# Performance work log

Hardware: AMD Instinct MI355X
Metric: run time of the kernel (lower is better)

The kernel has to match this reference:

```python
import jax, jax.numpy as jnp
import numpy as np
from jax import lax

TOP_K = 4
ROUTED_SCALING = 1.0
RENORMALIZE = True


def setup_inputs() -> dict:
    key = jax.random.key(0)
    ks = jax.random.split(key, 9)
    H, I, E = 2048, 1024, 16
    s = 0.02
    return {
        "hidden_states": jax.random.normal(ks[0], (2, 1024, H), jnp.float32),
        "gate_w": jax.random.normal(ks[1], (E, H), jnp.float32) * s,
        "expert_bias": jax.random.normal(ks[2], (E,), jnp.float32) * s,
        "w_gate": jax.random.normal(ks[3], (E, I, H), jnp.float32) * s,
        "w_up": jax.random.normal(ks[4], (E, I, H), jnp.float32) * s,
        "w_down": jax.random.normal(ks[5], (E, H, I), jnp.float32) * s,
        "sw_gate": jax.random.normal(ks[6], (I, H), jnp.float32) * s,
        "sw_up": jax.random.normal(ks[7], (I, H), jnp.float32) * s,
        "sw_down": jax.random.normal(ks[8], (H, I), jnp.float32) * s,
    }


def _swiglu_ffn(x, wg, wu, wd):
    # SiluAndMul(gate_up) -> down_proj
    return (jax.nn.silu(x @ wg.T) * (x @ wu.T)) @ wd.T


def reference(hidden_states, gate_w, expert_bias, w_gate, w_up, w_down,
              sw_gate, sw_up, sw_down):
    orig_shape = hidden_states.shape
    H = orig_shape[-1]
    x = hidden_states.reshape(-1, H)            # [T, H]
    T = x.shape[0]

    # --- sigmoid gating with score-correction bias (bias affects selection only) ---
    logits = x.astype(jnp.float32) @ gate_w.T    # [T, E] fp32 router
    scores = jax.nn.sigmoid(logits)
    _, topk_idx = lax.top_k(scores + expert_bias[None, :], TOP_K)   # [T, K]
    topk_w = jnp.take_along_axis(scores, topk_idx, axis=-1)         # raw scores
    if RENORMALIZE:
        topk_w = topk_w / jnp.sum(topk_w, axis=-1, keepdims=True)
    topk_w = topk_w * ROUTED_SCALING

    # scatter top-k weights into dense [T, E] combine matrix
    E = gate_w.shape[0]
    combine = jnp.zeros((T, E), dtype=x.dtype).at[
        jnp.arange(T)[:, None], topk_idx].set(topk_w.astype(x.dtype))

    # --- routed experts: scan over experts, weighted accumulate ---
    def step(acc, ws):
        wg, wu, wd, cw = ws                     # cw: [T] combine weights
        return acc + cw[:, None] * _swiglu_ffn(x, wg, wu, wd), None

    routed, _ = lax.scan(step, jnp.zeros_like(x),
                         (w_gate, w_up, w_down, combine.T))

    # --- shared expert ---
    shared = _swiglu_ffn(x, sw_gate, sw_up, sw_down)

    return (routed + shared).reshape(orig_shape)
```

## Files before the change

kernel.cpp:

```cpp
#include <hip/hip_runtime.h>
#include <hip/hip_bf16.h>
#include <cstdint>

#define TK 2048
#define HD 2048
#define ID 1024
#define NE 16
#define NG 17
#define TOPK 4
#define SLOTS (TK*TOPK)
#define ROWS_ALL (SLOTS+TK)
#define IH (ID*HD)
#define MAXT 96
#define MAXTR 80

typedef __attribute__((ext_vector_type(4))) float f32x4;
typedef __attribute__((ext_vector_type(16))) float f32x16;
typedef __attribute__((ext_vector_type(8))) short s16x8;
typedef unsigned short u16;
typedef unsigned long long u64;

__device__ __forceinline__ u16 f2bf(float f){
  union { float f; uint32_t u; } v; v.f = f;
  uint32_t r = v.u + 0x7fffu + ((v.u >> 16) & 1u);
  return (u16)(r >> 16);
}

#define GLD16(g, l) __builtin_amdgcn_global_load_lds( \
    (const __attribute__((address_space(1))) void*)(g), \
    (__attribute__((address_space(3))) void*)(l), 16, 0, 0)

__device__ __forceinline__ const s16x8* fragp(const u16* b, int row, int off){
  return (const s16x8*)((const char*)b + row*128 + (off ^ ((row&7)<<4)));
}

#define MFMA32(a,b,c) __builtin_amdgcn_mfma_f32_32x32x16_bf16((a),(b),(c),0,0,0)

__global__ void k_prep(const float* __restrict__ x, u16* __restrict__ xb,
                       u64* __restrict__ maskbits){
  int gi = blockIdx.x*blockDim.x + threadIdx.x;
  int st = gridDim.x*blockDim.x;
  if (gi < NE*32) maskbits[gi] = 0ull;
  for (int i=gi; i<TK*HD/4; i+=st){
    float4 f = ((const float4*)x)[i];
    ushort4 o; o.x=f2bf(f.x); o.y=f2bf(f.y); o.z=f2bf(f.z); o.w=f2bf(f.w);
    ((ushort4*)xb)[i] = o;
  }
}

__global__ void k_cvtw(const float* __restrict__ wg, const float* __restrict__ wu,
                       const float* __restrict__ wd, const float* __restrict__ swg,
                       const float* __restrict__ swu, const float* __restrict__ swd,
                       u16* __restrict__ wgb, u16* __restrict__ wub, u16* __restrict__ wdb){
  const size_t nbig = (size_t)NE*IH/4, nsml = IH/4;
  const size_t total = 3*nbig + 3*nsml;
  for (size_t i = (size_t)blockIdx.x*blockDim.x + threadIdx.x; i < total;
       i += (size_t)gridDim.x*blockDim.x){
    const float4* src; ushort4* dst; size_t j = i;
    if (j < nbig){ src=(const float4*)wg + j;  dst=(ushort4*)wgb + j; }
    else if ((j-=nbig) < nbig){ src=(const float4*)wu + j;  dst=(ushort4*)wub + j; }
    else if ((j-=nbig) < nbig){ src=(const float4*)wd + j;  dst=(ushort4*)wdb + j; }
    else if ((j-=nbig) < nsml){ src=(const float4*)swg + j; dst=(ushort4*)wgb + nbig + j; }
    else if ((j-=nsml) < nsml){ src=(const float4*)swu + j; dst=(ushort4*)wub + nbig + j; }
    else { j-=nsml; src=(const float4*)swd + j; dst=(ushort4*)wdb + nbig + j; }
    float4 f = *src;
    ushort4 o; o.x=f2bf(f.x); o.y=f2bf(f.y); o.z=f2bf(f.z); o.w=f2bf(f.w);
    *dst = o;
  }
}

__global__ __launch_bounds__(256) void k_logits(const float* __restrict__ x,
                                                const float* __restrict__ gw,
                                                const float* __restrict__ bias,
                                                float* __restrict__ wdense,
                                                u64* __restrict__ maskbits){
  int t = blockIdx.x, tid = threadIdx.x;
  int lane = tid & 63, wv = tid >> 6;
  const float* xr = x + (size_t)t*HD;
  float acc[NE];
  #pragma unroll
  for (int e=0;e<NE;e++) acc[e]=0.f;
  for (int k=tid;k<HD;k+=256){
    float xv = xr[k];
    #pragma unroll
    for (int e=0;e<NE;e++) acc[e] += xv * gw[e*HD + k];
  }
  __shared__ float red[NE][4];
  #pragma unroll
  for (int e=0;e<NE;e++){
    float v = acc[e];
    #pragma unroll
    for (int off=32;off>0;off>>=1) v += __shfl_down(v, off, 64);
    if (lane==0) red[e][wv] = v;
  }
  __syncthreads();
  if (tid == 0){
    float sc[NE], bs[NE];
    #pragma unroll
    for (int e=0;e<NE;e++){
      float l = red[e][0]+red[e][1]+red[e][2]+red[e][3];
      float s = 1.f/(1.f+expf(-l));
      sc[e]=s; bs[e]=s+bias[e];
    }
    int idx[TOPK]; float wsum=0.f; unsigned used=0;
    for (int k=0;k<TOPK;k++){
      int best=0; float bv=-1e30f;
      for (int e=0;e<NE;e++) if (!((used>>e)&1u) && bs[e] > bv){ bv=bs[e]; best=e; }
      used |= 1u<<best; idx[k]=best; wsum += sc[best];
    }
    float inv = 1.f/wsum;
    for (int k=0;k<TOPK;k++){
      int e = idx[k];
      wdense[t*NE + e] = sc[e]*inv;
      atomicOr(&maskbits[e*32 + (t>>6)], 1ull << (t&63));
    }
  }
}

__global__ void k_scan(const u64* __restrict__ maskbits, int* __restrict__ counts,
                       int* __restrict__ offsets, int* __restrict__ wordpfx,
                       int* __restrict__ tiles, int* __restrict__ tilesR){
  int acc = 0;
  for (int e=0;e<NE;e++){
    int c = 0;
    for (int w=0;w<32;w++){ wordpfx[e*32+w] = c; c += __popcll(maskbits[e*32+w]); }
    counts[e] = c;
  }
  for (int e=0;e<NE;e++){ offsets[e] = acc; acc += counts[e]; }
  offsets[NE] = acc;
  counts[NE] = TK;
  int nt = 0, nr = 0;
  for (int g=0; g<NG; g++){
    int c = counts[g];
    for (int mt=0; mt*128 < c; mt++){
      if (nt < MAXT) tiles[nt++] = (g<<8) | mt;
      if (g < NE && nr < MAXTR) tilesR[nr++] = (g<<8) | mt;
    }
  }
  for (; nt<MAXT;  nt++) tiles[nt]  = -1;
  for (; nr<MAXTR; nr++) tilesR[nr] = -1;
}

__global__ void k_scatter(const u64* __restrict__ maskbits, const int* __restrict__ offsets,
                          const int* __restrict__ wordpfx, const float* __restrict__ wdense,
                          int* __restrict__ rowtok, float* __restrict__ roww){
  int t = blockIdx.x*blockDim.x + threadIdx.x;
  int e = blockIdx.y;
  if (t >= TK) return;
  if (e == NE){ rowtok[offsets[NE]+t] = t; roww[offsets[NE]+t] = 1.f; return; }
  u64 w = maskbits[e*32 + (t>>6)];
  if ((w >> (t&63)) & 1ull){
    int pos = offsets[e] + wordpfx[e*32 + (t>>6)] + __popcll(w & ((1ull << (t&63)) - 1ull));
    rowtok[pos] = t; roww[pos] = wdense[t*NE + e];
  }
}

__global__ __launch_bounds__(256, 2) void k_gemm1b(
    const u16* __restrict__ xb, const u16* __restrict__ wgb, const u16* __restrict__ wub,
    const int* __restrict__ counts, const int* __restrict__ offsets,
    const int* __restrict__ rowtok, const float* __restrict__ roww,
    const int* __restrict__ tiles, u16* __restrict__ P)
{
  int te = tiles[blockIdx.y];
  if (te < 0) return;
  int g = te >> 8, mt = te & 255;
  int cnt = counts[g];
  int n0 = blockIdx.x*128;
  int base = offsets[g];
  const u16* wg16 = wgb + (size_t)g*IH;
  const u16* wu16 = wub + (size_t)g*IH;

  __shared__ u16 lsA[128*64];
  __shared__ u16 lsG[128*64];
  __shared__ u16 lsU[128*64];

  int tid = threadIdx.x, lane = tid & 63, wv = tid >> 6;
  int wm = (wv>>1)*64, wn64 = (wv&1)*64;
  int rl = lane & 31, hi = lane >> 5;

  f32x16 accg[2][2] = {}; f32x16 accu[2][2] = {};

  const u16 *aSrc[4], *gSrc[4], *uSrc[4];
  #pragma unroll
  for (int i=0;i<4;i++){
    int b = i*256 + tid, r = b>>3, cb = b&7;
    int m = mt*128 + r; if (m >= cnt) m = cnt-1;
    int tok = rowtok[base + m];
    aSrc[i] = xb + (size_t)tok*HD + ((cb ^ (r&7))<<3);
    size_t woff = (size_t)(n0 + r)*HD + ((cb ^ (r&7))<<3);
    gSrc[i] = wg16 + woff; uSrc[i] = wu16 + woff;
  }

  for (int t=0; t<HD/64; ++t){
    int k0 = t*64;
    #pragma unroll
    for (int i=0;i<4;i++) GLD16(aSrc[i]+k0, lsA + (i*256 + wv*64)*8);
    #pragma unroll
    for (int i=0;i<4;i++) GLD16(gSrc[i]+k0, lsG + (i*256 + wv*64)*8);
    #pragma unroll
    for (int i=0;i<4;i++) GLD16(uSrc[i]+k0, lsU + (i*256 + wv*64)*8);
    asm volatile("s_waitcnt vmcnt(0)" ::: "memory");
    __builtin_amdgcn_s_barrier();
    #pragma unroll
    for (int s=0; s<4; ++s){
      int off = s*32 + hi*16;
      s16x8 af[2], bg[2], bu[2];
      af[0] = *fragp(lsA, wm + rl, off);
      af[1] = *fragp(lsA, wm + 32 + rl, off);
      bg[0] = *fragp(lsG, wn64 + rl, off);
      bg[1] = *fragp(lsG, wn64 + 32 + rl, off);
      bu[0] = *fragp(lsU, wn64 + rl, off);
      bu[1] = *fragp(lsU, wn64 + 32 + rl, off);
      #pragma unroll
      for (int mi=0;mi<2;mi++){
        #pragma unroll
        for (int j=0;j<2;j++){
          accg[mi][j] = MFMA32(af[mi], bg[j], accg[mi][j]);
          accu[mi][j] = MFMA32(af[mi], bu[j], accu[mi][j]);
        }
      }
    }
    asm volatile("s_waitcnt lgkmcnt(0)" ::: "memory");
    __builtin_amdgcn_s_barrier();
  }
  #pragma unroll
  for (int mi=0;mi<2;mi++){
    #pragma unroll
    for (int r=0;r<16;r++){
      int rowb = wm + mi*32 + (r&3) + 8*(r>>2) + 4*hi;
      int m = mt*128 + rowb;
      if (m < cnt){
        int slot = base + m;
        float wgt = roww[slot];
        #pragma unroll
        for (int j=0;j<2;j++){
          float gv = accg[mi][j][r], uv = accu[mi][j][r];
          float pv = gv/(1.f+expf(-gv))*uv*wgt;
          P[(size_t)slot*ID + n0 + wn64 + j*32 + rl] = f2bf(pv);
        }
      }
    }
  }
}

template<bool ATOMIC>
__global__ __launch_bounds__(256, 2) void k_gemm2b(
    const u16* __restrict__ P, const u16* __restrict__ wdb,
    const int* __restrict__ counts, const int* __restrict__ offsets,
    const int* __restrict__ rowtok, const int* __restrict__ tiles,
    float* __restrict__ out)
{
  int g, mt, cnt, base;
  if (ATOMIC){
    int te = tiles[blockIdx.y];
    if (te < 0) return;
    g = te >> 8; mt = te & 255; cnt = counts[g]; base = offsets[g];
  } else {
    g = NE; mt = blockIdx.y; cnt = TK; base = SLOTS;
  }
  int n0 = blockIdx.x*256;
  const u16* wd16 = wdb + (size_t)g*IH;

  __shared__ u16 lsA[128*64];
  __shared__ u16 lsB[256*64];

  int tid = threadIdx.x, lane = tid & 63, wv = tid >> 6;
  int wm = (wv>>1)*64, wn = (wv&1)*128;
  int rl = lane & 31, hi = lane >> 5;
  f32x16 acc[2][4] = {};

  const u16* aSrc[4];
  #pragma unroll
  for (int i=0;i<4;i++){
    int b = i*256 + tid, r = b>>3, cb = b&7;
    int m = mt*128 + r; if (m >= cnt) m = cnt-1;
    aSrc[i] = P + (size_t)(base + m)*ID + ((cb ^ (r&7))<<3);
  }
  const u16* bSrc[8];
  #pragma unroll
  for (int i=0;i<8;i++){
    int b = i*256 + tid, r = b>>3, cb = b&7;
    bSrc[i] = wd16 + (size_t)(n0 + r)*ID + ((cb ^ (r&7))<<3);
  }

  for (int t=0; t<ID/64; ++t){
    int k0 = t*64;
    #pragma unroll
    for (int i=0;i<4;i++) GLD16(aSrc[i]+k0, lsA + (i*256 + wv*64)*8);
    #pragma unroll
    for (int i=0;i<8;i++) GLD16(bSrc[i]+k0, lsB + (i*256 + wv*64)*8);
    asm volatile("s_waitcnt vmcnt(0)" ::: "memory");
    __builtin_amdgcn_s_barrier();
    #pragma unroll
    for (int s=0; s<4; ++s){
      int off = s*32 + hi*16;
      s16x8 af[2], bf[4];
      af[0] = *fragp(lsA, wm + rl, off);
      af[1] = *fragp(lsA, wm + 32 + rl, off);
      #pragma unroll
      for (int nj=0;nj<4;nj++) bf[nj] = *fragp(lsB, wn + nj*32 + rl, off);
      #pragma unroll
      for (int mi=0;mi<2;mi++)
        #pragma unroll
        for (int nj=0;nj<4;nj++)
          acc[mi][nj] = MFMA32(af[mi], bf[nj], acc[mi][nj]);
    }
    asm volatile("s_waitcnt lgkmcnt(0)" ::: "memory");
    __builtin_amdgcn_s_barrier();
  }
  #pragma unroll
  for (int mi=0;mi<2;mi++){
    #pragma unroll
    for (int r=0;r<16;r++){
      int rowb = wm + mi*32 + (r&3) + 8*(r>>2) + 4*hi;
      int m = mt*128 + rowb;
      if (m < cnt){
        int tok = rowtok[base + m];
        float* orow = out + (size_t)tok*HD + n0 + wn + rl;
        #pragma unroll
        for (int nj=0;nj<4;nj++){
          if (ATOMIC) atomicAdd(orow + nj*32, acc[mi][nj][r]);
          else        orow[nj*32] = acc[mi][nj][r];
        }
      }
    }
  }
}


extern "C" void kernel_launch(void* const* d_in, const int* in_sizes, int n_in,
                              void* d_out, int out_size, void* d_ws, size_t ws_size,
                              hipStream_t stream){
  (void)in_sizes; (void)n_in; (void)ws_size; (void)out_size;
  const float* x       = (const float*)d_in[0];
  const float* gate_w  = (const float*)d_in[1];
  const float* ebias   = (const float*)d_in[2];
  const float* w_gate  = (const float*)d_in[3];
  const float* w_up    = (const float*)d_in[4];
  const float* w_down  = (const float*)d_in[5];
  const float* sw_gate = (const float*)d_in[6];
  const float* sw_up   = (const float*)d_in[7];
  const float* sw_down = (const float*)d_in[8];
  float* out = (float*)d_out;

  char* p = (char*)d_ws;
  auto alloc = [&](size_t bytes)->char*{ char* r = p; p += (bytes + 255) & ~(size_t)255; return r; };
  u16*   xb       = (u16*)  alloc((size_t)TK*HD*2);
  u16*   P        = (u16*)  alloc((size_t)ROWS_ALL*ID*2);
  float* wdense   = (float*)alloc((size_t)TK*NE*4);
  u64*   maskbits = (u64*)  alloc((size_t)NE*32*8);
  int*   wordpfx  = (int*)  alloc((size_t)NE*32*4);
  int*   counts   = (int*)  alloc(64);
  int*   offsets  = (int*)  alloc(64);
  int*   tiles    = (int*)  alloc(MAXT*4);
  int*   tilesR   = (int*)  alloc(MAXTR*4);
  int*   rowtok   = (int*)  alloc((size_t)ROWS_ALL*4);
  float* roww     = (float*)alloc((size_t)ROWS_ALL*4);
  size_t slab = (size_t)NG*IH*2;
  u16* wgb = (u16*)alloc(slab);
  u16* wub = (u16*)alloc(slab);
  u16* wdb = (u16*)alloc(slab);

  k_prep<<<2048, 256, 0, stream>>>(x, xb, maskbits);
  k_cvtw<<<2048, 256, 0, stream>>>(w_gate, w_up, w_down, sw_gate, sw_up, sw_down,
                                   wgb, wub, wdb);
  k_logits<<<TK, 256, 0, stream>>>(x, gate_w, ebias, wdense, maskbits);
  k_scan<<<1, 1, 0, stream>>>(maskbits, counts, offsets, wordpfx, tiles, tilesR);
  k_scatter<<<dim3(TK/256, NG), 256, 0, stream>>>(maskbits, offsets, wordpfx, wdense, rowtok, roww);

  dim3 g1(ID/128, MAXT);
  k_gemm1b<<<g1, 256, 0, stream>>>(xb, wgb, wub, counts, offsets, rowtok, roww, tiles, P);
  dim3 g2s(HD/256, TK/128);
  k_gemm2b<false><<<g2s, 256, 0, stream>>>(P, wdb, counts, offsets, rowtok, nullptr, out);
  dim3 g2r(HD/256, MAXTR);
  k_gemm2b<true ><<<g2r, 256, 0, stream>>>(P, wdb, counts, offsets, rowtok, tilesR, out);
}
```

Measured before the change: 461.5 us.

## Replace atomic down-proj scatter with bf16 per-slot outputs plus gather-reduce kernel

```diff
diff --git a/kernel.cpp b/kernel.cpp
--- a/kernel.cpp
+++ b/kernel.cpp
@@ -12,7 +12,6 @@
 #define ROWS_ALL (SLOTS+TK)
 #define IH (ID*HD)
 #define MAXT 96
-#define MAXTR 80
 
 typedef __attribute__((ext_vector_type(4))) float f32x4;
 typedef __attribute__((ext_vector_type(16))) float f32x16;
@@ -30,17 +29,21 @@
     (const __attribute__((address_space(1))) void*)(g), \
     (__attribute__((address_space(3))) void*)(l), 16, 0, 0)
 
+__device__ __forceinline__ int swz(int r){
+  return (r & 7) ^ (((r >> 3) & 3) << 1);
+}
 __device__ __forceinline__ const s16x8* fragp(const u16* b, int row, int off){
-  return (const s16x8*)((const char*)b + row*128 + (off ^ ((row&7)<<4)));
+  return (const s16x8*)((const char*)b + row*128 + (off ^ (swz(row)<<4)));
 }
 
 #define MFMA32(a,b,c) __builtin_amdgcn_mfma_f32_32x32x16_bf16((a),(b),(c),0,0,0)
 
 __global__ void k_prep(const float* __restrict__ x, u16* __restrict__ xb,
-                       u64* __restrict__ maskbits){
+                       u64* __restrict__ maskbits, int* __restrict__ tokcnt){
   int gi = blockIdx.x*blockDim.x + threadIdx.x;
   int st = gridDim.x*blockDim.x;
   if (gi < NE*32) maskbits[gi] = 0ull;
+  if (gi < TK) tokcnt[gi] = 0;
   for (int i=gi; i<TK*HD/4; i+=st){
     float4 f = ((const float4*)x)[i];
     ushort4 o; o.x=f2bf(f.x); o.y=f2bf(f.y); o.z=f2bf(f.z); o.w=f2bf(f.w);
@@ -119,7 +122,7 @@
 
 __global__ void k_scan(const u64* __restrict__ maskbits, int* __restrict__ counts,
                        int* __restrict__ offsets, int* __restrict__ wordpfx,
-                       int* __restrict__ tiles, int* __restrict__ tilesR){
+                       int* __restrict__ tiles){
   int acc = 0;
   for (int e=0;e<NE;e++){
     int c = 0;
@@ -129,21 +132,18 @@
   for (int e=0;e<NE;e++){ offsets[e] = acc; acc += counts[e]; }
   offsets[NE] = acc;
   counts[NE] = TK;
-  int nt = 0, nr = 0;
+  int nt = 0;
   for (int g=0; g<NG; g++){
     int c = counts[g];
-    for (int mt=0; mt*128 < c; mt++){
-      if (nt < MAXT) tiles[nt++] = (g<<8) | mt;
-      if (g < NE && nr < MAXTR) tilesR[nr++] = (g<<8) | mt;
-    }
-  }
-  for (; nt<MAXT;  nt++) tiles[nt]  = -1;
-  for (; nr<MAXTR; nr++) tilesR[nr] = -1;
+    for (int mt=0; mt*128 < c && nt < MAXT; mt++) tiles[nt++] = (g<<8) | mt;
+  }
+  for (; nt<MAXT; nt++) tiles[nt] = -1;
 }
 
 __global__ void k_scatter(const u64* __restrict__ maskbits, const int* __restrict__ offsets,
                           const int* __restrict__ wordpfx, const float* __restrict__ wdense,
-                          int* __restrict__ rowtok, float* __restrict__ roww){
+                          int* __restrict__ rowtok, float* __restrict__ roww,
+                          int* __restrict__ tokcnt, int* __restrict__ tok4){
   int t = blockIdx.x*blockDim.x + threadIdx.x;
   int e = blockIdx.y;
   if (t >= TK) return;
@@ -152,6 +152,8 @@
   if ((w >> (t&63)) & 1ull){
     int pos = offsets[e] + wordpfx[e*32 + (t>>6)] + __popcll(w & ((1ull << (t&63)) - 1ull));
     rowtok[pos] = t; roww[pos] = wdense[t*NE + e];
+    int r = atomicAdd(&tokcnt[t], 1);
+    tok4[t*TOPK + r] = pos;
   }
 }
 
@@ -186,8 +188,8 @@
     int b = i*256 + tid, r = b>>3, cb = b&7;
     int m = mt*128 + r; if (m >= cnt) m = cnt-1;
     int tok = rowtok[base + m];
-    aSrc[i] = xb + (size_t)tok*HD + ((cb ^ (r&7))<<3);
-    size_t woff = (size_t)(n0 + r)*HD + ((cb ^ (r&7))<<3);
+    aSrc[i] = xb + (size_t)tok*HD + ((cb ^ swz(r))<<3);
+    size_t woff = (size_t)(n0 + r)*HD + ((cb ^ swz(r))<<3);
     gSrc[i] = wg16 + woff; uSrc[i] = wu16 + woff;
   }
 
@@ -243,21 +245,16 @@
   }
 }
 
-template<bool ATOMIC>
 __global__ __launch_bounds__(256, 2) void k_gemm2b(
     const u16* __restrict__ P, const u16* __restrict__ wdb,
     const int* __restrict__ counts, const int* __restrict__ offsets,
-    const int* __restrict__ rowtok, const int* __restrict__ tiles,
-    float* __restrict__ out)
+    const int* __restrict__ tiles, u16* __restrict__ R)
 {
-  int g, mt, cnt, base;
-  if (ATOMIC){
-    int te = tiles[blockIdx.y];
-    if (te < 0) return;
-    g = te >> 8; mt = te & 255; cnt = counts[g]; base = offsets[g];
-  } else {
-    g = NE; mt = blockIdx.y; cnt = TK; base = SLOTS;
-  }
+  int te = tiles[blockIdx.y];
+  if (te < 0) return;
+  int g = te >> 8, mt = te & 255;
+  int cnt = counts[g];
+  int base = offsets[g];
   int n0 = blockIdx.x*256;
   const u16* wd16 = wdb + (size_t)g*IH;
 
@@ -274,13 +271,13 @@
   for (int i=0;i<4;i++){
     int b = i*256 + tid, r = b>>3, cb = b&7;
     int m = mt*128 + r; if (m >= cnt) m = cnt-1;
-    aSrc[i] = P + (size_t)(base + m)*ID + ((cb ^ (r&7))<<3);
+    aSrc[i] = P + (size_t)(base + m)*ID + ((cb ^ swz(r))<<3);
   }
   const u16* bSrc[8];
   #pragma unroll
   for (int i=0;i<8;i++){
     int b = i*256 + tid, r = b>>3, cb = b&7;
-    bSrc[i] = wd16 + (size_t)(n0 + r)*ID + ((cb ^ (r&7))<<3);
+    bSrc[i] = wd16 + (size_t)(n0 + r)*ID + ((cb ^ swz(r))<<3);
   }
 
   for (int t=0; t<ID/64; ++t){
@@ -315,14 +312,41 @@
       int rowb = wm + mi*32 + (r&3) + 8*(r>>2) + 4*hi;
       int m = mt*128 + rowb;
       if (m < cnt){
-        int tok = rowtok[base + m];
-        float* orow = out + (size_t)tok*HD + n0 + wn + rl;
+        u16* rrow = R + (size_t)(base + m)*HD + n0 + wn + rl;
         #pragma unroll
-        for (int nj=0;nj<4;nj++){
-          if (ATOMIC) atomicAdd(orow + nj*32, acc[mi][nj][r]);
-          else        orow[nj*32] = acc[mi][nj][r];
-        }
+        for (int nj=0;nj<4;nj++) rrow[nj*32] = f2bf(acc[mi][nj][r]);
       }
+    }
+  }
+}
+
+__global__ __launch_bounds__(256) void k_reduce(const u16* __restrict__ R,
+                                                const int* __restrict__ tok4,
+                                                float* __restrict__ out){
+  int t = blockIdx.x;
+  int c0 = threadIdx.x * 8;
+  int s0 = tok4[t*TOPK+0], s1 = tok4[t*TOPK+1], s2 = tok4[t*TOPK+2], s3 = tok4[t*TOPK+3];
+  const ushort4* p0 = (const ushort4*)(R + (size_t)s0*HD + c0);
+  const ushort4* p1 = (const ushort4*)(R + (size_t)s1*HD + c0);
+  const ushort4* p2 = (const ushort4*)(R + (size_t)s2*HD + c0);
+  const ushort4* p3 = (const ushort4*)(R + (size_t)s3*HD + c0);
+  const ushort4* ps = (const ushort4*)(R + (size_t)(SLOTS + t)*HD + c0);
+  float* o = out + (size_t)t*HD + c0;
+  #pragma unroll
+  for (int h=0; h<2; h++){
+    ushort4 a = p0[h], b = p1[h], c = p2[h], d = p3[h], e = ps[h];
+    #pragma unroll
+    for (int j=0;j<4;j++){
+      u16 ua = ((const u16*)&a)[j], ub = ((const u16*)&b)[j];
+      u16 uc = ((const u16*)&c)[j], ud = ((const u16*)&d)[j], ue = ((const u16*)&e)[j];
+      float v = ((float)(int)0);
+      union { uint32_t u; float f; } w;
+      w.u = (uint32_t)ua<<16; v  = w.f;
+      w.u = (uint32_t)ub<<16; v += w.f;
+      w.u = (uint32_t)uc<<16; v += w.f;
+      w.u = (uint32_t)ud<<16; v += w.f;
+      w.u = (uint32_t)ue<<16; v += w.f;
+      o[h*4 + j] = v;
     }
   }
 }
@@ -353,25 +377,27 @@
   int*   counts   = (int*)  alloc(64);
   int*   offsets  = (int*)  alloc(64);
   int*   tiles    = (int*)  alloc(MAXT*4);
-  int*   tilesR   = (int*)  alloc(MAXTR*4);
   int*   rowtok   = (int*)  alloc((size_t)ROWS_ALL*4);
   float* roww     = (float*)alloc((size_t)ROWS_ALL*4);
+  int*   tokcnt   = (int*)  alloc((size_t)TK*4);
+  int*   tok4     = (int*)  alloc((size_t)TK*TOPK*4);
   size_t slab = (size_t)NG*IH*2;
   u16* wgb = (u16*)alloc(slab);
   u16* wub = (u16*)alloc(slab);
   u16* wdb = (u16*)alloc(slab);
-
-  k_prep<<<2048, 256, 0, stream>>>(x, xb, maskbits);
+  u16* R = wgb;
+
+  k_prep<<<2048, 256, 0, stream>>>(x, xb, maskbits, tokcnt);
   k_cvtw<<<2048, 256, 0, stream>>>(w_gate, w_up, w_down, sw_gate, sw_up, sw_down,
                                    wgb, wub, wdb);
   k_logits<<<TK, 256, 0, stream>>>(x, gate_w, ebias, wdense, maskbits);
-  k_scan<<<1, 1, 0, stream>>>(maskbits, counts, offsets, wordpfx, tiles, tilesR);
-  k_scatter<<<dim3(TK/256, NG), 256, 0, stream>>>(maskbits, offsets, wordpfx, wdense, rowtok, roww);
+  k_scan<<<1, 1, 0, stream>>>(maskbits, counts, offsets, wordpfx, tiles);
+  k_scatter<<<dim3(TK/256, NG), 256, 0, stream>>>(maskbits, offsets, wordpfx, wdense,
+                                                  rowtok, roww, tokcnt, tok4);
 
   dim3 g1(ID/128, MAXT);
   k_gemm1b<<<g1, 256, 0, stream>>>(xb, wgb, wub, counts, offsets, rowtok, roww, tiles, P);
-  dim3 g2s(HD/256, TK/128);
-  k_gemm2b<false><<<g2s, 256, 0, stream>>>(P, wdb, counts, offsets, rowtok, nullptr, out);
-  dim3 g2r(HD/256, MAXTR);
-  k_gemm2b<true ><<<g2r, 256, 0, stream>>>(P, wdb, counts, offsets, rowtok, tilesR, out);
-}
+  dim3 g2(HD/256, MAXT);
+  k_gemm2b<<<g2, 256, 0, stream>>>(P, wdb, counts, offsets, tiles, R);
+  k_reduce<<<TK, 256, 0, stream>>>(R, tok4, out);
+}
```

Result: faster. 393.2 us (-14.8%).
